# Kernel tuning notes

Hardware: AMD Instinct MI355X
Metric: run time of the kernel (lower is better)

## Reference

```python
import jax, jax.numpy as jnp
import numpy as np

T = 4096        # sequence length
D = 128         # input feature dim
TRACE = 64      # trace_size
CONTEXT = 64    # context_size
HID = 64        # internal dense width (hardcoded 64 in module)
OUT = 128       # output_size
LN_EPS = 1e-6   # flax LayerNorm default epsilon


def setup_inputs() -> dict:
    key = jax.random.key(0)
    ks = jax.random.split(key, 12)

    def dense(k, fi, fo):
        return (jax.random.normal(k, (fi, fo), jnp.float32) / np.sqrt(fi).astype(np.float32))

    inp = {}
    inp["x"] = jax.random.normal(ks[0], (T, D), jnp.float32)
    inp["state"] = jnp.zeros((1, TRACE, CONTEXT), jnp.complex64)
    inp["start"] = jax.random.uniform(ks[1], (T,)) < 0.01  # sparse episode resets
    # deterministic FFM decay / frequency params (init_deterministic)
    inp["a"] = jnp.linspace(1e-6, 0.5, TRACE).astype(jnp.float32)
    inp["b"] = (2.0 * jnp.pi / jnp.linspace(1.0, 1000.0, CONTEXT)).astype(jnp.float32)
    inp["W1"] = dense(ks[2], D, HID);               inp["b1"] = jnp.zeros((HID,), jnp.float32)
    inp["W2"] = dense(ks[3], HID, 2 * TRACE);       inp["b2"] = jnp.zeros((2 * TRACE,), jnp.float32)
    inp["Wgi"] = dense(ks[4], 2 * TRACE, TRACE);    inp["bgi"] = jnp.zeros((TRACE,), jnp.float32)
    inp["Wp"] = dense(ks[5], 2 * TRACE, TRACE);     inp["bp"] = jnp.zeros((TRACE,), jnp.float32)
    inp["Wz"] = dense(ks[6], 2 * TRACE * CONTEXT, HID); inp["bz"] = jnp.zeros((HID,), jnp.float32)
    inp["Wgo"] = dense(ks[7], 2 * TRACE, HID);      inp["bgo"] = jnp.zeros((HID,), jnp.float32)
    inp["Ws"] = dense(ks[8], 2 * TRACE, HID);       inp["bs"] = jnp.zeros((HID,), jnp.float32)
    inp["W3"] = dense(ks[9], HID, HID);             inp["b3"] = jnp.zeros((HID,), jnp.float32)
    inp["W4"] = dense(ks[10], HID, OUT);            inp["b4"] = jnp.zeros((OUT,), jnp.float32)
    return inp


def _ffm_scan(scan_in, state0, start, a, b):
    # scan_in: (T, TRACE, CONTEXT) float, state0: (1, TRACE, CONTEXT) complex64
    t = scan_in.shape[0]
    timestep = jnp.ones((t + 1, 1, 1), dtype=jnp.int32)
    start_f = jnp.concatenate(
        [jnp.zeros((1, 1, 1), dtype=bool), start.reshape(t, 1, 1)], axis=0)
    xs = jnp.concatenate([state0, scan_in.astype(jnp.complex64)], axis=0)

    neg_a = -jnp.abs(a).reshape(1, TRACE, 1)
    b_r = b.reshape(1, 1, CONTEXT)
    ab = neg_a + 1j * b_r  # (1, TRACE, CONTEXT) complex

    def gamma(j):
        # j: (N,1,1) int -> (N, TRACE, CONTEXT) complex decay
        return jnp.exp(ab * j.astype(jnp.float32))

    def combine(carry, incoming):
        prev_start, s, i = carry
        st, xx, j = incoming
        keep = jnp.logical_not(st)
        s = s * keep
        j = j * keep.astype(j.dtype)
        new_s = s * gamma(j) + xx
        return (jnp.logical_or(st, prev_start), new_s, j + i)

    _, new_state, _ = jax.lax.associative_scan(
        combine, (start_f, xs, timestep), axis=0)
    return new_state[1:]  # (T, TRACE, CONTEXT) complex64


def _layernorm(x):
    mu = jnp.mean(x, axis=-1, keepdims=True)
    var = jnp.var(x, axis=-1, keepdims=True)
    return (x - mu) * jax.lax.rsqrt(var + LN_EPS)


def _forward(x, state, start, a, b, W1, b1, W2, b2, Wgi, bgi, Wp, bp,
             Wz, bz, Wgo, bgo, Ws, bs, W3, b3, W4, b4):
    h = jax.nn.relu(x @ W1 + b1)                 # (T, 64)
    h2 = h @ W2 + b2                             # (T, 2*TRACE)
    gate_in = jax.nn.sigmoid(h2 @ Wgi + bgi)     # (T, TRACE)
    pre = jax.nn.sigmoid(h2 @ Wp + bp)           # (T, TRACE)
    gated = pre * gate_in                        # (T, TRACE)
    scan_in = jnp.broadcast_to(gated[:, :, None], (gated.shape[0], TRACE, CONTEXT))
    state_seq = _ffm_scan(scan_in, state, start, a, b)  # (T, TRACE, CONTEXT) c64
    z_in = jnp.concatenate([jnp.real(state_seq), jnp.imag(state_seq)],
                           axis=-1).reshape(state_seq.shape[0], -1)
    z = z_in @ Wz + bz                           # (T, 64)
    gate_out = jax.nn.sigmoid(h2 @ Wgo + bgo)    # (T, 64)
    skip = h2 @ Ws + bs                          # (T, 64)
    out = _layernorm(z * gate_out) + skip * (1.0 - gate_out)
    out = jax.nn.relu(out @ W3 + b3)
    out = out @ W4 + b4                          # (T, OUT)
    return out, state_seq[-1:]


def reference(x, state, start, a, b, W1, b1, W2, b2, Wgi, bgi, Wp, bp,
              Wz, bz, Wgo, bgo, Ws, bs, W3, b3, W4, b4):
    return _forward(x, state, start, a, b, W1, b1, W2, b2, Wgi, bgi, Wp, bp,
                    Wz, bz, Wgo, bgo, Ws, bs, W3, b3, W4, b4)
```

## Files before the change

### kernel.cpp

```cpp
#include <hip/hip_runtime.h>
#include <math.h>

#define T_LEN 4096
#define D_IN 128
#define KDIM 4096
#define K2   8192

#define OFF_GATED 0u
#define OFF_GO    262144u
#define OFF_SKIP  524288u
#define OFF_PART  786432u
#define OFF_FLAGS 4980736u
#define OFF_CHS   4984832u
#define OFF_WZT   4984896u
#define OFF_SCR   5247040u

typedef __attribute__((ext_vector_type(8))) short short8v;
typedef __attribute__((ext_vector_type(4))) float float4v;

__device__ __forceinline__ float sigm(float x){ return 1.f/(1.f+expf(-x)); }
__device__ __forceinline__ unsigned short f2bf(float x){
    unsigned int u = __float_as_uint(x);
    return (unsigned short)((u + 0x7FFFu + ((u >> 16) & 1u)) >> 16);
}
__device__ __forceinline__ float wsum(float v) {
#pragma unroll
    for (int o = 32; o; o >>= 1) v += __shfl_xor(v, o, 64);
    return v;
}

__global__ __launch_bounds__(512) void k_prep(
    const unsigned char* __restrict__ su8, const int* __restrict__ si32,
    int* __restrict__ flags, int* __restrict__ chunkStart,
    const float* __restrict__ Wz, unsigned short* __restrict__ wzt,
    const float* __restrict__ x,
    const float* __restrict__ W1, const float* __restrict__ b1,
    const float* __restrict__ W2, const float* __restrict__ b2,
    const float* __restrict__ Wgi, const float* __restrict__ bgi,
    const float* __restrict__ Wp,  const float* __restrict__ bp,
    const float* __restrict__ Wgo, const float* __restrict__ bgo,
    const float* __restrict__ Wsk, const float* __restrict__ bsk,
    float* __restrict__ gated, float* __restrict__ go, float* __restrict__ sk)
{
    const int bx = blockIdx.x;
    const int tid = threadIdx.x;

    if (bx == 0) {
        __shared__ int cnt;
        if (tid == 0) cnt = 0;
        __syncthreads();
        int local = 0;
        for (int i = tid; i < 4096; i += 512)
            if (i & 3) local += su8[i];
        if (local) atomicAdd(&cnt, local);
        __syncthreads();
        if (cnt > 0) { for (int i = tid; i < 4096; i += 512) flags[i] = su8[i] ? 1 : 0; }
        else         { for (int i = tid; i < 4096; i += 512) flags[i] = si32[i] ? 1 : 0; }
        __syncthreads();
        if (tid < 64) {
            int any = 0;
#pragma unroll 8
            for (int j = 0; j < 64; ++j) any |= flags[tid * 64 + j];
            chunkStart[tid] = any;
        }
        return;
    }
    if (bx <= 64) {
        int idx = ((bx - 1) * 512 + tid) * 16;
        int j = idx >> 13, k0 = idx & 8191;
#pragma unroll
        for (int e = 0; e < 16; ++e) {
            int k = k0 + e;
            wzt[(size_t)j * K2 + k] = f2bf(Wz[(size_t)k * 64 + j]);
        }
        return;
    }

    __shared__ float xs[8][128];
    __shared__ float hs[8][64];
    __shared__ float h2s[8][128];
    __shared__ float tmp[8][4][64];
    const int t0 = (bx - 65) * 8;

    if (tid < 256) {
        int r = tid >> 5, kq = (tid & 31) << 2;
        *(float4*)&xs[r][kq] = *(const float4*)&x[(size_t)(t0 + r) * D_IN + kq];
    }

    const int j1 = tid >> 3, ks1 = tid & 7;
    float wr1[16];
#pragma unroll
    for (int kk = 0; kk < 16; ++kk) wr1[kk] = W1[(size_t)(ks1 * 16 + kk) * 64 + j1];
    const float bias1 = b1[j1];
    __syncthreads();
#pragma unroll
    for (int r = 0; r < 8; ++r) {
        float p = 0.f;
#pragma unroll
        for (int kq = 0; kq < 4; ++kq) {
            float4 xv = *(const float4*)&xs[r][ks1 * 16 + kq * 4];
            p += xv.x*wr1[kq*4] + xv.y*wr1[kq*4+1] + xv.z*wr1[kq*4+2] + xv.w*wr1[kq*4+3];
        }
        p += __shfl_xor(p, 1, 64); p += __shfl_xor(p, 2, 64); p += __shfl_xor(p, 4, 64);
        if (ks1 == 0) hs[r][j1] = fmaxf(p + bias1, 0.f);
    }
    __syncthreads();

    const int j2 = tid >> 2, ks2 = tid & 3;
    float wr2[16];
#pragma unroll
    for (int kk = 0; kk < 16; ++kk) wr2[kk] = W2[(size_t)(ks2 * 16 + kk) * 128 + j2];
    const float bias2 = b2[j2];
#pragma unroll
    for (int r = 0; r < 8; ++r) {
        float p = 0.f;
#pragma unroll
        for (int kq = 0; kq < 4; ++kq) {
            float4 hv = *(const float4*)&hs[r][ks2 * 16 + kq * 4];
            p += hv.x*wr2[kq*4] + hv.y*wr2[kq*4+1] + hv.z*wr2[kq*4+2] + hv.w*wr2[kq*4+3];
        }
        p += __shfl_xor(p, 1, 64); p += __shfl_xor(p, 2, 64);
        if (ks2 == 0) h2s[r][j2] = p + bias2;
    }
    __syncthreads();

    const int mat = tid >> 7, jj = (tid & 127) >> 1, kh = tid & 1;
    const float* Wm = (mat == 0) ? Wgi : (mat == 1) ? Wp : (mat == 2) ? Wgo : Wsk;
    float wgr[64];
#pragma unroll
    for (int kk = 0; kk < 64; ++kk) wgr[kk] = Wm[(size_t)(kh * 64 + kk) * 64 + jj];
#pragma unroll
    for (int r = 0; r < 8; ++r) {
        float p = 0.f;
#pragma unroll
        for (int kq = 0; kq < 16; ++kq) {
            float4 hv = *(const float4*)&h2s[r][kh * 64 + kq * 4];
            p += hv.x*wgr[kq*4] + hv.y*wgr[kq*4+1] + hv.z*wgr[kq*4+2] + hv.w*wgr[kq*4+3];
        }
        p += __shfl_xor(p, 1, 64);
        if (kh == 0) tmp[r][mat][jj] = p;
    }
    __syncthreads();

    {
        int r = tid >> 6, j = tid & 63;
        int t = t0 + r;
        float gi = sigm(tmp[r][0][j] + bgi[j]);
        float pr = sigm(tmp[r][1][j] + bp[j]);
        float g  = sigm(tmp[r][2][j] + bgo[j]);
        float s  = tmp[r][3][j] + bsk[j];
        gated[t * 64 + j] = gi * pr;
        go[t * 64 + j]    = g;
        sk[t * 64 + j]    = s;
    }
}

__global__ __launch_bounds__(512) void k_scanA(
    const float* __restrict__ gated, const int* __restrict__ flags,
    const float* __restrict__ a, const float* __restrict__ b,
    float2* __restrict__ carryB)
{
    const int p = threadIdx.x >> 6, c = threadIdx.x & 63;
    const int pair = blockIdx.x * 8 + p;
    const int ch = pair & 63, m = pair >> 6;
    const int t0 = ch * 64;

    const double ea = exp(-fabs((double)a[m]));
    const double bb = (double)b[c];
    const double lre = ea * cos(bb), lim = ea * sin(bb);
    float gv = gated[(size_t)(t0 + c) * 64 + m];
    unsigned long long fmask = __ballot(flags[t0 + c] != 0);
    double sre = 0.0, sim = 0.0;
#pragma unroll 8
    for (int j = 0; j < 64; ++j) {
        double g = (double)__shfl(gv, j, 64);
        if ((fmask >> j) & 1) { sre = g; sim = 0.0; }
        else {
            double nr = fma(sre, lre, fma(-sim, lim, g));
            double ni = fma(sre, lim, sim * lre);
            sre = nr; sim = ni;
        }
    }
    carryB[(size_t)ch * KDIM + m * 64 + c] = make_float2((float)sre, (float)sim);
}

__global__ __launch_bounds__(256) void k_scanBZq(
    const float* __restrict__ gated, const int* __restrict__ flags,
    const int* __restrict__ chs,
    const float* __restrict__ a, const float* __restrict__ b,
    const float* __restrict__ st0,
    const float2* __restrict__ carryB,
    const unsigned short* __restrict__ wzt,
    float* __restrict__ part,
    float* __restrict__ out)
{
    const int tid = threadIdx.x;
    const int ml = tid >> 6, c = tid & 63;
    const int ch = blockIdx.x & 63, mg = blockIdx.x >> 6;
    const int m = mg * 4 + ml;
    const int t0 = ch * 64;
    __shared__ unsigned short st[64 * 512];

    const double ea = exp(-fabs((double)a[m]));
    const double bb = (double)b[c];
    const double lre = ea * cos(bb), lim = ea * sin(bb);

    unsigned long long cmask = __ballot(chs[c] != 0);
    const double ea64 = exp(-64.0 * fabs((double)a[m]));
    const double l64re = ea64 * cos(64.0 * bb), l64im = ea64 * sin(64.0 * bb);
    double cre = (double)st0[(m * 64 + c) * 2];
    double cim = (double)st0[(m * 64 + c) * 2 + 1];
    {
        const float2* cbase = carryB + m * 64 + c;
        float2 BA[16], BB[16];
#define LOADB(dst, base)                                          \
        _Pragma("unroll")                                         \
        for (int q = 0; q < 16; ++q)                              \
            dst[q] = cbase[(size_t)((base) + q) * KDIM];
#define COMB(src, base)                                           \
        _Pragma("unroll")                                         \
        for (int q = 0; q < 16; ++q) {                            \
            int chp = (base) + q;                                 \
            if (chp < ch) {       \
                if ((cmask >> chp) & 1) { cre = (double)src[q].x; cim = (double)src[q].y; } \
                else {                                            \
                    double nr = fma(cre, l64re, fma(-cim, l64im, (double)src[q].x)); \
                    double ni = fma(cre, l64im, fma(cim, l64re, (double)src[q].y)); \
                    cre = nr; cim = ni;                           \
                }                                                 \
            }                                                     \
        }
        if (ch > 0)  { LOADB(BA, 0) }
        if (ch > 16) { LOADB(BB, 16) }
        if (ch > 0)  { COMB(BA, 0) }
        if (ch > 32) { LOADB(BA, 32) }
        if (ch > 16) { COMB(BB, 16) }
        if (ch > 48) { LOADB(BB, 48) }
        if (ch > 32) { COMB(BA, 32) }
        if (ch > 48) { COMB(BB, 48) }
#undef LOADB
#undef COMB
    }

    float gv = gated[(size_t)(t0 + c) * 64 + m];
    unsigned long long fmask = __ballot(flags[t0 + c] != 0);
    double sre = cre, sim = cim;
    const int e0 = ml * 128 + c, e1 = e0 + 64;
#pragma unroll 4
    for (int j = 0; j < 64; ++j) {
        double g = (double)__shfl(gv, j, 64);
        if ((fmask >> j) & 1) { sre = g; sim = 0.0; }
        else {
            double nr = fma(sre, lre, fma(-sim, lim, g));
            double ni = fma(sre, lim, sim * lre);
            sre = nr; sim = ni;
        }
        const int sx = (j & 7) << 3;
        st[j * 512 + (e0 ^ sx)] = f2bf((float)sre);
        st[j * 512 + (e1 ^ sx)] = f2bf((float)sim);
    }
    if (ch == 63) {
        out[524288 + m * 64 + c]        = (float)sre;
        out[524288 + 4096 + m * 64 + c] = (float)sim;
    }

    const int l = c;
    const int jrow = ml * 16 + (l & 15);
    short8v bfr[16];
#pragma unroll
    for (int ks = 0; ks < 16; ++ks)
        bfr[ks] = *(const short8v*)&wzt[(size_t)jrow * K2 + mg * 512 + (ks * 4 + (l >> 4)) * 8];

    __syncthreads();

    float4v acc[4];
#pragma unroll
    for (int i = 0; i < 4; ++i) acc[i] = (float4v){0.f, 0.f, 0.f, 0.f};
#pragma unroll
    for (int ks = 0; ks < 16; ++ks) {
#pragma unroll
        for (int mt = 0; mt < 4; ++mt) {
            const int row = mt * 16 + (l & 15);
            const int rchunk = (ks * 4 + (l >> 4)) ^ (row & 7);
            short8v af = *(const short8v*)&st[row * 512 + rchunk * 8];
            acc[mt] = __builtin_amdgcn_mfma_f32_16x16x32_bf16(af, bfr[ks], acc[mt], 0, 0, 0);
        }
    }

    float* pp = part + (size_t)mg * 262144;
    const int jcol = ml * 16 + (l & 15);
#pragma unroll
    for (int mt = 0; mt < 4; ++mt) {
        const int trow = t0 + mt * 16 + (l >> 4) * 4;
#pragma unroll
        for (int r = 0; r < 4; ++r)
            pp[(size_t)(trow + r) * 64 + jcol] = acc[mt][r];
    }
}

__global__ __launch_bounds__(256) void k_epi(
    const float* __restrict__ part, const float* __restrict__ bz,
    const float* __restrict__ go, const float* __restrict__ sk,
    const float* __restrict__ W3, const float* __restrict__ b3,
    const float* __restrict__ W4, const float* __restrict__ b4,
    float* __restrict__ out)
{
    __shared__ float ob[4][64], hb[4][64];
    const int w = threadIdx.x >> 6, j = threadIdx.x & 63;
    const int t = blockIdx.x * 4 + w;
    float z = bz[j];
#pragma unroll
    for (int p = 0; p < 16; ++p) z += part[(size_t)p * 262144 + t * 64 + j];
    float g = go[t * 64 + j];
    float y = z * g;
    float mu = wsum(y) * 0.015625f;
    float d = y - mu;
    float var = wsum(d * d) * 0.015625f;
    float o = d * (1.f / sqrtf(var + 1e-6f)) + sk[t * 64 + j] * (1.f - g);
    ob[w][j] = o;
    __syncthreads();
    float acc = b3[j];
#pragma unroll 8
    for (int k = 0; k < 64; ++k) acc += ob[w][k] * W3[k * 64 + j];
    hb[w][j] = fmaxf(acc, 0.f);
    __syncthreads();
    float o1 = b4[j], o2 = b4[j + 64];
#pragma unroll 8
    for (int k = 0; k < 64; ++k) { float hv = hb[w][k]; o1 += hv * W4[k * 128 + j]; o2 += hv * W4[k * 128 + j + 64]; }
    out[(size_t)t * 128 + j] = o1;
    out[(size_t)t * 128 + j + 64] = o2;
}

extern "C" void kernel_launch(void* const* d_in, const int* in_sizes, int n_in,
                              void* d_out, int out_size, void* d_ws, size_t ws_size,
                              hipStream_t stream)
{
    const float* x   = (const float*)d_in[0];
    const float* st0 = (const float*)d_in[1];
    const void*  start = d_in[2];
    const float* a  = (const float*)d_in[3];
    const float* b  = (const float*)d_in[4];
    const float* W1 = (const float*)d_in[5];  const float* b1 = (const float*)d_in[6];
    const float* W2 = (const float*)d_in[7];  const float* b2 = (const float*)d_in[8];
    const float* Wgi= (const float*)d_in[9];  const float* bgi= (const float*)d_in[10];
    const float* Wp = (const float*)d_in[11]; const float* bp = (const float*)d_in[12];
    const float* Wz = (const float*)d_in[13]; const float* bz = (const float*)d_in[14];
    const float* Wgo= (const float*)d_in[15]; const float* bgo= (const float*)d_in[16];
    const float* Wsk= (const float*)d_in[17]; const float* bsk= (const float*)d_in[18];
    const float* W3 = (const float*)d_in[19]; const float* b3 = (const float*)d_in[20];
    const float* W4 = (const float*)d_in[21]; const float* b4 = (const float*)d_in[22];

    float* ws    = (float*)d_ws;
    float* out   = (float*)d_out;
    float* gated = ws + OFF_GATED;
    float* go    = ws + OFF_GO;
    float* sk    = ws + OFF_SKIP;
    float* part  = ws + OFF_PART;
    int*   flags = (int*)(ws + OFF_FLAGS);
    int*   chs   = (int*)(ws + OFF_CHS);
    unsigned short* wzt = (unsigned short*)(ws + OFF_WZT);
    float2* carryB = (float2*)(ws + OFF_SCR);

    hipLaunchKernelGGL(k_prep, dim3(577), dim3(512), 0, stream,
                       (const unsigned char*)start, (const int*)start, flags, chs,
                       Wz, wzt, x, W1, b1, W2, b2, Wgi, bgi, Wp, bp,
                       Wgo, bgo, Wsk, bsk, gated, go, sk);
    hipLaunchKernelGGL(k_scanA, dim3(512), dim3(512), 0, stream,
                       gated, flags, a, b, carryB);
    hipLaunchKernelGGL(k_scanBZq, dim3(1024), dim3(256), 0, stream,
                       gated, flags, chs, a, b, st0, carryB, wzt, part, out);
    hipLaunchKernelGGL(k_epi, dim3(1024), dim3(256), 0, stream,
                       part, bz, go, sk, W3, b3, W4, b4, out);
}
```

Baseline: 86.43 us.

## Switch scan recurrences to fp32 and process two chunks per scanBZ block

The chunked scan recurrences in k_scanA and the fused scan+Wz kernel now run in single precision instead of double, which is much cheaper on the vector ALUs. The fused kernel also handles two consecutive 64-step chunks per block, so the carry combine and the Wz fragment loads into registers are amortized over twice the work, and the grid is halved. The trade-offs are reduced accuracy in the long-range recurrence and fewer blocks for latency hiding.

```diff
diff --git a/kernel.cpp b/kernel.cpp
--- a/kernel.cpp
+++ b/kernel.cpp
@@ -165,26 +165,26 @@
     const int ch = pair & 63, m = pair >> 6;
     const int t0 = ch * 64;
 
-    const double ea = exp(-fabs((double)a[m]));
-    const double bb = (double)b[c];
-    const double lre = ea * cos(bb), lim = ea * sin(bb);
+    const double ead = exp(-fabs((double)a[m]));
+    const double bbd = (double)b[c];
+    const float lre = (float)(ead * cos(bbd)), lim = (float)(ead * sin(bbd));
     float gv = gated[(size_t)(t0 + c) * 64 + m];
     unsigned long long fmask = __ballot(flags[t0 + c] != 0);
-    double sre = 0.0, sim = 0.0;
+    float sre = 0.f, sim = 0.f;
 #pragma unroll 8
     for (int j = 0; j < 64; ++j) {
-        double g = (double)__shfl(gv, j, 64);
-        if ((fmask >> j) & 1) { sre = g; sim = 0.0; }
+        float g = __shfl(gv, j, 64);
+        if ((fmask >> j) & 1) { sre = g; sim = 0.f; }
         else {
-            double nr = fma(sre, lre, fma(-sim, lim, g));
-            double ni = fma(sre, lim, sim * lre);
+            float nr = fmaf(sre, lre, fmaf(-sim, lim, g));
+            float ni = fmaf(sre, lim, sim * lre);
             sre = nr; sim = ni;
         }
     }
-    carryB[(size_t)ch * KDIM + m * 64 + c] = make_float2((float)sre, (float)sim);
-}
-
-__global__ __launch_bounds__(256) void k_scanBZq(
+    carryB[(size_t)ch * KDIM + m * 64 + c] = make_float2(sre, sim);
+}
+
+__global__ __launch_bounds__(256) void k_scanBZ2(
     const float* __restrict__ gated, const int* __restrict__ flags,
     const int* __restrict__ chs,
     const float* __restrict__ a, const float* __restrict__ b,
@@ -196,20 +196,21 @@
 {
     const int tid = threadIdx.x;
     const int ml = tid >> 6, c = tid & 63;
-    const int ch = blockIdx.x & 63, mg = blockIdx.x >> 6;
+    const int chpair = blockIdx.x & 31, mg = blockIdx.x >> 5;
+    const int ch0 = chpair * 2;
     const int m = mg * 4 + ml;
-    const int t0 = ch * 64;
     __shared__ unsigned short st[64 * 512];
 
-    const double ea = exp(-fabs((double)a[m]));
-    const double bb = (double)b[c];
-    const double lre = ea * cos(bb), lim = ea * sin(bb);
+    const double ead = exp(-fabs((double)a[m]));
+    const double bbd = (double)b[c];
+    const float lre = (float)(ead * cos(bbd)), lim = (float)(ead * sin(bbd));
 
     unsigned long long cmask = __ballot(chs[c] != 0);
     const double ea64 = exp(-64.0 * fabs((double)a[m]));
-    const double l64re = ea64 * cos(64.0 * bb), l64im = ea64 * sin(64.0 * bb);
-    double cre = (double)st0[(m * 64 + c) * 2];
-    double cim = (double)st0[(m * 64 + c) * 2 + 1];
+    const float l64re = (float)(ea64 * cos(64.0 * bbd));
+    const float l64im = (float)(ea64 * sin(64.0 * bbd));
+    float cre = st0[(m * 64 + c) * 2];
+    float cim = st0[(m * 64 + c) * 2 + 1];
     {
         const float2* cbase = carryB + m * 64 + c;
         float2 BA[16], BB[16];
@@ -221,47 +222,25 @@
         _Pragma("unroll")                                         \
         for (int q = 0; q < 16; ++q) {                            \
             int chp = (base) + q;                                 \
-            if (chp < ch) {       \
-                if ((cmask >> chp) & 1) { cre = (double)src[q].x; cim = (double)src[q].y; } \
+            if (chp < ch0) {      \
+                if ((cmask >> chp) & 1) { cre = src[q].x; cim = src[q].y; } \
                 else {                                            \
-                    double nr = fma(cre, l64re, fma(-cim, l64im, (double)src[q].x)); \
-                    double ni = fma(cre, l64im, fma(cim, l64re, (double)src[q].y)); \
+                    float nr = fmaf(cre, l64re, fmaf(-cim, l64im, src[q].x)); \
+                    float ni = fmaf(cre, l64im, fmaf(cim, l64re, src[q].y)); \
                     cre = nr; cim = ni;                           \
                 }                                                 \
             }                                                     \
         }
-        if (ch > 0)  { LOADB(BA, 0) }
-        if (ch > 16) { LOADB(BB, 16) }
-        if (ch > 0)  { COMB(BA, 0) }
-        if (ch > 32) { LOADB(BA, 32) }
-        if (ch > 16) { COMB(BB, 16) }
-        if (ch > 48) { LOADB(BB, 48) }
-        if (ch > 32) { COMB(BA, 32) }
-        if (ch > 48) { COMB(BB, 48) }
+        if (ch0 > 0)  { LOADB(BA, 0) }
+        if (ch0 > 16) { LOADB(BB, 16) }
+        if (ch0 > 0)  { COMB(BA, 0) }
+        if (ch0 > 32) { LOADB(BA, 32) }
+        if (ch0 > 16) { COMB(BB, 16) }
+        if (ch0 > 48) { LOADB(BB, 48) }
+        if (ch0 > 32) { COMB(BA, 32) }
+        if (ch0 > 48) { COMB(BB, 48) }
 #undef LOADB
 #undef COMB
-    }
-
-    float gv = gated[(size_t)(t0 + c) * 64 + m];
-    unsigned long long fmask = __ballot(flags[t0 + c] != 0);
-    double sre = cre, sim = cim;
-    const int e0 = ml * 128 + c, e1 = e0 + 64;
-#pragma unroll 4
-    for (int j = 0; j < 64; ++j) {
-        double g = (double)__shfl(gv, j, 64);
-        if ((fmask >> j) & 1) { sre = g; sim = 0.0; }
-        else {
-            double nr = fma(sre, lre, fma(-sim, lim, g));
-            double ni = fma(sre, lim, sim * lre);
-            sre = nr; sim = ni;
-        }
-        const int sx = (j & 7) << 3;
-        st[j * 512 + (e0 ^ sx)] = f2bf((float)sre);
-        st[j * 512 + (e1 ^ sx)] = f2bf((float)sim);
-    }
-    if (ch == 63) {
-        out[524288 + m * 64 + c]        = (float)sre;
-        out[524288 + 4096 + m * 64 + c] = (float)sim;
     }
 
     const int l = c;
@@ -271,30 +250,56 @@
     for (int ks = 0; ks < 16; ++ks)
         bfr[ks] = *(const short8v*)&wzt[(size_t)jrow * K2 + mg * 512 + (ks * 4 + (l >> 4)) * 8];
 
-    __syncthreads();
-
-    float4v acc[4];
-#pragma unroll
-    for (int i = 0; i < 4; ++i) acc[i] = (float4v){0.f, 0.f, 0.f, 0.f};
-#pragma unroll
-    for (int ks = 0; ks < 16; ++ks) {
+    const int e0 = ml * 128 + c, e1 = e0 + 64;
+    const int jcol = ml * 16 + (l & 15);
+
+    for (int u = 0; u < 2; ++u) {
+        const int ch = ch0 + u, t0s = ch * 64;
+
+        float gv = gated[(size_t)(t0s + c) * 64 + m];
+        unsigned long long fmask = __ballot(flags[t0s + c] != 0);
+#pragma unroll 4
+        for (int j = 0; j < 64; ++j) {
+            float g = __shfl(gv, j, 64);
+            if ((fmask >> j) & 1) { cre = g; cim = 0.f; }
+            else {
+                float nr = fmaf(cre, lre, fmaf(-cim, lim, g));
+                float ni = fmaf(cre, lim, cim * lre);
+                cre = nr; cim = ni;
+            }
+            const int sx = (j & 7) << 3;
+            st[j * 512 + (e0 ^ sx)] = f2bf(cre);
+            st[j * 512 + (e1 ^ sx)] = f2bf(cim);
+        }
+        if (ch == 63) {
+            out[524288 + m * 64 + c]        = cre;
+            out[524288 + 4096 + m * 64 + c] = cim;
+        }
+        __syncthreads();
+
+        float4v acc[4];
+#pragma unroll
+        for (int i = 0; i < 4; ++i) acc[i] = (float4v){0.f, 0.f, 0.f, 0.f};
+#pragma unroll
+        for (int ks = 0; ks < 16; ++ks) {
+#pragma unroll
+            for (int mt = 0; mt < 4; ++mt) {
+                const int row = mt * 16 + (l & 15);
+                const int rchunk = (ks * 4 + (l >> 4)) ^ (row & 7);
+                short8v af = *(const short8v*)&st[row * 512 + rchunk * 8];
+                acc[mt] = __builtin_amdgcn_mfma_f32_16x16x32_bf16(af, bfr[ks], acc[mt], 0, 0, 0);
+            }
+        }
+
+        float* pp = part + (size_t)mg * 262144;
 #pragma unroll
         for (int mt = 0; mt < 4; ++mt) {
-            const int row = mt * 16 + (l & 15);
-            const int rchunk = (ks * 4 + (l >> 4)) ^ (row & 7);
-            short8v af = *(const short8v*)&st[row * 512 + rchunk * 8];
-            acc[mt] = __builtin_amdgcn_mfma_f32_16x16x32_bf16(af, bfr[ks], acc[mt], 0, 0, 0);
-        }
-    }
-
-    float* pp = part + (size_t)mg * 262144;
-    const int jcol = ml * 16 + (l & 15);
-#pragma unroll
-    for (int mt = 0; mt < 4; ++mt) {
-        const int trow = t0 + mt * 16 + (l >> 4) * 4;
-#pragma unroll
-        for (int r = 0; r < 4; ++r)
-            pp[(size_t)(trow + r) * 64 + jcol] = acc[mt][r];
+            const int trow = t0s + mt * 16 + (l >> 4) * 4;
+#pragma unroll
+            for (int r = 0; r < 4; ++r)
+                pp[(size_t)(trow + r) * 64 + jcol] = acc[mt][r];
+        }
+        __syncthreads();
     }
 }
 
@@ -367,7 +372,7 @@
                        Wgo, bgo, Wsk, bsk, gated, go, sk);
     hipLaunchKernelGGL(k_scanA, dim3(512), dim3(512), 0, stream,
                        gated, flags, a, b, carryB);
-    hipLaunchKernelGGL(k_scanBZq, dim3(1024), dim3(256), 0, stream,
+    hipLaunchKernelGGL(k_scanBZ2, dim3(512), dim3(256), 0, stream,
                        gated, flags, chs, a, b, st0, carryB, wzt, part, out);
     hipLaunchKernelGGL(k_epi, dim3(1024), dim3(256), 0, stream,
                        part, bz, go, sk, W3, b3, W4, b4, out);
```

Measured after the change: 76.71 us, median of 2. 1.13x faster.
